# Kernel tuning notes

Hardware: AMD Instinct MI355X
Metric: run time of the kernel (lower is better)

The kernel has to match this reference:

```python
import jax, jax.numpy as jnp
import numpy as np

B, T, IN, H, OUT, HOR = 512, 720, 6, 128, 3, 360


def _cell(xin, h, c, Wih, Whh, bih, bhh):
    # PyTorch LSTM gate order: i, f, g, o
    g = xin @ Wih.T + h @ Whh.T + bih + bhh
    i, f, gg, o = jnp.split(g, 4, axis=-1)
    c = jax.nn.sigmoid(f) * c + jax.nn.sigmoid(i) * jnp.tanh(gg)
    h = jax.nn.sigmoid(o) * jnp.tanh(c)
    return h, c


def _run_layer(x, Wih, Whh, bih, bhh, reverse):
    xs = x[:, ::-1] if reverse else x
    # hoist input projection out of the scan: (B,T,4H)
    pre = jnp.einsum('bti,gi->btg', xs, Wih) + bih + bhh
    h0 = jnp.zeros((x.shape[0], Whh.shape[1]), x.dtype)

    def step(carry, gt):
        h, c = carry
        g = gt + h @ Whh.T
        i, f, gg, o = jnp.split(g, 4, axis=-1)
        c = jax.nn.sigmoid(f) * c + jax.nn.sigmoid(i) * jnp.tanh(gg)
        h = jax.nn.sigmoid(o) * jnp.tanh(c)
        return (h, c), h

    (hT, cT), ys = jax.lax.scan(step, (h0, h0), jnp.swapaxes(pre, 0, 1))
    ys = jnp.swapaxes(ys, 0, 1)
    if reverse:
        ys = ys[:, ::-1]
    return ys, hT, cT


def reference(x, e0f_Wih, e0f_Whh, e0f_bih, e0f_bhh, e0b_Wih, e0b_Whh, e0b_bih, e0b_bhh,
              e1f_Wih, e1f_Whh, e1f_bih, e1f_bhh, e1b_Wih, e1b_Whh, e1b_bih, e1b_bhh,
              brh_W, brh_b, brc_W, brc_b,
              d0_Wih, d0_Whh, d0_bih, d0_bhh, d1_Wih, d1_Whh, d1_bih, d1_bhh,
              out_W, out_b, start_token):
    b = x.shape[0]
    # bidirectional encoder, layer 0 (input_dim -> H per direction)
    y0f, h0f, c0f = _run_layer(x, e0f_Wih, e0f_Whh, e0f_bih, e0f_bhh, False)
    y0b, h0b, c0b = _run_layer(x, e0b_Wih, e0b_Whh, e0b_bih, e0b_bhh, True)
    y0 = jnp.concatenate([y0f, y0b], axis=-1)  # (B,T,2H)
    # layer 1 (2H -> H per direction); dropout inactive in eval
    _, h1f, c1f = _run_layer(y0, e1f_Wih, e1f_Whh, e1f_bih, e1f_bhh, False)
    _, h1b, c1b = _run_layer(y0, e1b_Wih, e1b_Whh, e1b_bih, e1b_bhh, True)
    # (num_layers, B, 2H): cat fwd/bwd final states per layer
    h_enc = jnp.stack([jnp.concatenate([h0f, h0b], -1), jnp.concatenate([h1f, h1b], -1)])
    c_enc = jnp.stack([jnp.concatenate([c0f, c0b], -1), jnp.concatenate([c1f, c1b], -1)])
    h_dec = h_enc @ brh_W.T + brh_b  # (2,B,H)
    c_dec = c_enc @ brc_W.T + brc_b
    xin0 = jnp.broadcast_to(start_token[0, 0], (b, start_token.shape[-1]))  # (B,3)

    def dec_step(carry, _):
        h0, c0, h1, c1, xin = carry
        h0, c0 = _cell(xin, h0, c0, d0_Wih, d0_Whh, d0_bih, d0_bhh)
        h1, c1 = _cell(h0, h1, c1, d1_Wih, d1_Whh, d1_bih, d1_bhh)
        pred = h1 @ out_W.T + out_b
        return (h0, c0, h1, c1, pred), pred

    carry0 = (h_dec[0], c_dec[0], h_dec[1], c_dec[1], xin0)
    _, preds = jax.lax.scan(dec_step, carry0, None, length=HOR)  # (HOR,B,3)
    return jnp.swapaxes(preds, 0, 1)  # (B,HOR,3)


def setup_inputs() -> dict:
    ks = iter(jax.random.split(jax.random.key(0), 40))

    def p(shape, s=0.05):
        return jax.random.normal(next(ks), shape, dtype=jnp.float32) * s

    d = {"x": jax.random.normal(next(ks), (B, T, IN), dtype=jnp.float32)}
    for name, ind in (("e0f", IN), ("e0b", IN), ("e1f", 2 * H), ("e1b", 2 * H)):
        d[name + "_Wih"] = p((4 * H, ind))
        d[name + "_Whh"] = p((4 * H, H))
        d[name + "_bih"] = p((4 * H,))
        d[name + "_bhh"] = p((4 * H,))
    d["brh_W"] = p((H, 2 * H)); d["brh_b"] = p((H,))
    d["brc_W"] = p((H, 2 * H)); d["brc_b"] = p((H,))
    for name, ind in (("d0", OUT), ("d1", H)):
        d[name + "_Wih"] = p((4 * H, ind))
        d[name + "_Whh"] = p((4 * H, H))
        d[name + "_bih"] = p((4 * H,))
        d[name + "_bhh"] = p((4 * H,))
    d["out_W"] = p((OUT, H)); d["out_b"] = p((OUT,))
    d["start_token"] = p((1, 1, OUT), 0.01)
    return d
```

## Files before the change

kernel.cpp:

```cpp
#include <hip/hip_runtime.h>

typedef __attribute__((ext_vector_type(8))) short bf16x8;
typedef __attribute__((ext_vector_type(4))) float f32x4;

#define MFMA16(a,b,c) __builtin_amdgcn_mfma_f32_16x16x32_bf16((a),(b),(c),0,0,0)

#define T_SEQ  720
#define NB     512
#define HD     128
#define GD     512
#define BT     16
#define HP     136
#define HP0    168
#define YT     256
#define WLP    68
#define HORZ   360

__device__ __forceinline__ float bf2f_(unsigned short u){
  union { unsigned int i; float f; } v; v.i = ((unsigned int)u) << 16; return v.f;
}
__device__ __forceinline__ unsigned short f2bf(float f){
  union { float f; unsigned int i; } v; v.f = f;
  unsigned int r = v.i + 0x7fffu + ((v.i >> 16) & 1u);
  return (unsigned short)(r >> 16);
}
__device__ __forceinline__ float rcp_(float x){ return __builtin_amdgcn_rcpf(x); }
__device__ __forceinline__ float sigm(float x){ return rcp_(1.f + __expf(-x)); }
__device__ __forceinline__ float tanh_(float x){
  return __builtin_fmaf(2.f, rcp_(1.f + __expf(-2.f * x)), -1.f);
}
__device__ __forceinline__ bf16x8 cvt8(const float* p){
  bf16x8 r;
  #pragma unroll
  for (int i = 0; i < 8; ++i) r[i] = (short)f2bf(p[i]);
  return r;
}
__device__ __forceinline__ void gl_lds16(const unsigned short* g, unsigned short* l){
  __builtin_amdgcn_global_load_lds(
      (const __attribute__((address_space(1))) void*)(g),
      (__attribute__((address_space(3))) void*)(l), 16, 0, 0);
}

__global__ __launch_bounds__(512, 2)
void enc_layer0_kernel(const float* __restrict__ x,
                       const float* __restrict__ WihF, const float* __restrict__ WhhF,
                       const float* __restrict__ bihF, const float* __restrict__ bhhF,
                       const float* __restrict__ WihB, const float* __restrict__ WhhB,
                       const float* __restrict__ bihB, const float* __restrict__ bhhB,
                       unsigned short* __restrict__ y0,
                       float* __restrict__ ench, float* __restrict__ encc)
{
  __shared__ __align__(16) unsigned short h_buf[2][BT * HP0];
  const int tid  = threadIdx.x;
  const int lane = tid & 63;
  const int w    = tid >> 6;
  const int l15  = lane & 15;
  const int q    = lane >> 4;
  const int dir  = blockIdx.x >> 5;
  const int bbase = (blockIdx.x & 31) * BT;

  const float* Wih = dir ? WihB : WihF;
  const float* Whh = dir ? WhhB : WhhF;
  const float* bih = dir ? bihB : bihF;
  const float* bhh = dir ? bhhB : bhhF;

  bf16x8 bw[4][5];
  f32x4  bias_vec[4];
  #pragma unroll
  for (int g = 0; g < 4; ++g) {
    const int n = g * 128 + w * 16 + l15;
    #pragma unroll
    for (int kt = 0; kt < 4; ++kt)
      bw[g][kt] = cvt8(Whh + n * HD + kt * 32 + q * 8);
    bf16x8 f;
    #pragma unroll
    for (int j = 0; j < 8; ++j) {
      const int kk = q * 8 + j;
      float wv = 0.f;
      if (kk < 6)       wv = Wih[n * 6 + kk];
      else if (kk < 12) wv = Wih[n * 6 + (kk - 6)];
      f[j] = (short)f2bf(wv);
    }
    bw[g][4] = f;
    const float b = bih[n] + bhh[n];
    bias_vec[g][0] = b; bias_vec[g][1] = b; bias_vec[g][2] = b; bias_vec[g][3] = b;
  }

  int t = dir ? (T_SEQ - 1) : 0;
  const int dt = dir ? -1 : 1;
  const int xr_ = tid / 6, xk_ = tid % 6;

  float cst[4] = {0.f, 0.f, 0.f, 0.f};
  for (int i = tid; i < 2 * BT * HP0; i += 512) (&h_buf[0][0])[i] = 0;
  __syncthreads();
  float xv_cur = 0.f;
  if (tid < 96) {
    const float v0 = x[((size_t)(bbase + xr_) * T_SEQ + t) * 6 + xk_];
    const unsigned short hi = f2bf(v0);
    h_buf[0][xr_ * HP0 + 128 + xk_] = hi;
    h_buf[0][xr_ * HP0 + 134 + xk_] = f2bf(v0 - bf2f_(hi));
    xv_cur = x[((size_t)(bbase + xr_) * T_SEQ + t + dt) * 6 + xk_];
  }
  __syncthreads();

  for (int s = 0; s < T_SEQ; ++s, t += dt) {
    const int cur = s & 1, nxt = cur ^ 1;

    if (s > 0 && tid < 256) {
      const int b = tid >> 4, c8 = tid & 15;
      const bf16x8 hv = *reinterpret_cast<const bf16x8*>(&h_buf[cur][b * HP0 + c8 * 8]);
      *reinterpret_cast<bf16x8*>(y0 + ((size_t)(bbase + b) * T_SEQ + (t - dt)) * 256 + dir * HD + c8 * 8) = hv;
    }
    float xv_next = 0.f;
    if (tid < 96 && s + 2 < T_SEQ)
      xv_next = x[((size_t)(bbase + xr_) * T_SEQ + (t + 2 * dt)) * 6 + xk_];

    f32x4 acc[4];
    #pragma unroll
    for (int kt = 0; kt < 5; ++kt) {
      const bf16x8 af = *reinterpret_cast<const bf16x8*>(&h_buf[cur][l15 * HP0 + kt * 32 + q * 8]);
      #pragma unroll
      for (int g = 0; g < 4; ++g)
        acc[g] = MFMA16(af, bw[g][kt], kt == 0 ? bias_vec[g] : acc[g]);
    }

    #pragma unroll
    for (int r = 0; r < 4; ++r) {
      const float i_ = acc[0][r], f_ = acc[1][r], g_ = acc[2][r], o_ = acc[3][r];
      const float c_ = sigm(f_) * cst[r] + sigm(i_) * tanh_(g_);
      cst[r] = c_;
      const float h_ = sigm(o_) * tanh_(c_);
      h_buf[nxt][(q * 4 + r) * HP0 + w * 16 + l15] = f2bf(h_);
      if (s == T_SEQ - 1) {
        const int b   = bbase + q * 4 + r;
        const int cix = w * 16 + l15;
        ench[(dir * NB + b) * HD + cix] = h_;
        encc[(dir * NB + b) * HD + cix] = c_;
      }
    }
    if (tid < 96 && s + 1 < T_SEQ) {
      const unsigned short hi = f2bf(xv_cur);
      h_buf[nxt][xr_ * HP0 + 128 + xk_] = hi;
      h_buf[nxt][xr_ * HP0 + 134 + xk_] = f2bf(xv_cur - bf2f_(hi));
    }
    xv_cur = xv_next;
    __syncthreads();
  }
  if (tid < 256) {
    const int cur = T_SEQ & 1;
    const int b = tid >> 4, c8 = tid & 15;
    const bf16x8 hv = *reinterpret_cast<const bf16x8*>(&h_buf[cur][b * HP0 + c8 * 8]);
    const int tl = dir ? 0 : (T_SEQ - 1);
    *reinterpret_cast<bf16x8*>(y0 + ((size_t)(bbase + b) * T_SEQ + tl) * 256 + dir * HD + c8 * 8) = hv;
  }
}

#define ENC1_YPART(ACC, YB)                                                    \
  {                                                                            \
    _Pragma("unroll")                                                          \
    for (int g = 0; g < 4; ++g) {                                              \
      (ACC)[g][0] = bias[g]; (ACC)[g][1] = bias[g];                            \
      (ACC)[g][2] = bias[g]; (ACC)[g][3] = bias[g];                            \
    }                                                                          \
    _Pragma("unroll")                                                          \
    for (int kt = 0; kt < 2; ++kt) {                                           \
      const int swz_ = ((kt * 4 + q) & 15) ^ l15;                              \
      const bf16x8 af = *reinterpret_cast<const bf16x8*>(&(YB)[l15 * YT + swz_ * 8]); \
      _Pragma("unroll")                                                        \
      for (int g = 0; g < 4; ++g) {                                            \
        const bf16x8 bl = *reinterpret_cast<const bf16x8*>(&wlds[nofs[g] + kt * 32 + q * 8]); \
        (ACC)[g] = MFMA16(af, bl, (ACC)[g]);                                   \
      }                                                                        \
    }                                                                          \
    _Pragma("unroll")                                                          \
    for (int kt = 2; kt < 8; ++kt) {                                           \
      const int c_ = kt * 4 + q;                                               \
      const int swz_ = (c_ & 16) | ((c_ & 15) ^ l15);                          \
      const bf16x8 af = *reinterpret_cast<const bf16x8*>(&(YB)[l15 * YT + swz_ * 8]); \
      _Pragma("unroll")                                                        \
      for (int g = 0; g < 4; ++g) (ACC)[g] = MFMA16(af, bw[g][kt - 2], (ACC)[g]); \
    }                                                                          \
  }

#define ENC1_BODY(S, CUR, NXT, ACCC, ACCN)                                     \
  {                                                                            \
    if ((S) + 2 < T_SEQ)                                                       \
      gl_lds16(y0 + grow + (size_t)(t + 2 * dt) * 256, b2 + w * 512);          \
    _Pragma("unroll")                                                          \
    for (int kt = 8; kt < 12; ++kt) {                                          \
      const bf16x8 af = *reinterpret_cast<const bf16x8*>(&h_buf[CUR][l15 * HP + (kt - 8) * 32 + q * 8]); \
      _Pragma("unroll")                                                        \
      for (int g = 0; g < 4; ++g) (ACCC)[g] = MFMA16(af, bw[g][kt - 2], (ACCC)[g]); \
    }                                                                          \
    if ((S) + 1 < T_SEQ) ENC1_YPART(ACCN, b1)                                  \
    _Pragma("unroll")                                                          \
    for (int r = 0; r < 4; ++r) {                                              \
      const float i_ = (ACCC)[0][r], f_ = (ACCC)[1][r];                        \
      const float g_ = (ACCC)[2][r], o_ = (ACCC)[3][r];                        \
      const float cc_ = sigm(f_) * cst[r] + sigm(i_) * tanh_(g_);              \
      cst[r] = cc_;                                                            \
      const float h_ = sigm(o_) * tanh_(cc_);                                  \
      h_buf[NXT][(q * 4 + r) * HP + w * 16 + l15] = f2bf(h_);                  \
      if ((S) == T_SEQ - 1) {                                                  \
        const int b_ = bbase + q * 4 + r;                                      \
        const int cix = w * 16 + l15;                                          \
        ench[(dir * NB + b_) * HD + cix] = h_;                                 \
        encc[(dir * NB + b_) * HD + cix] = cc_;                                \
      }                                                                        \
    }                                                                          \
    { unsigned short* tmp_ = b0; b0 = b1; b1 = b2; b2 = tmp_; }                \
    t += dt;                                                                   \
    __syncthreads();                                                           \
  }

__global__ __launch_bounds__(512, 2)
void enc_layer1_kernel(const unsigned short* __restrict__ y0,
                       const float* __restrict__ WihF, const float* __restrict__ WhhF,
                       const float* __restrict__ bihF, const float* __restrict__ bhhF,
                       const float* __restrict__ WihB, const float* __restrict__ WhhB,
                       const float* __restrict__ bihB, const float* __restrict__ bhhB,
                       float* __restrict__ ench, float* __restrict__ encc)
{
  __shared__ __align__(16) unsigned short wlds[GD * WLP];
  __shared__ __align__(16) unsigned short ybuf[3][BT * YT];
  __shared__ __align__(16) unsigned short h_buf[2][BT * HP];

  const int tid  = threadIdx.x;
  const int lane = tid & 63;
  const int w    = tid >> 6;
  const int l15  = lane & 15;
  const int q    = lane >> 4;
  const int dir  = blockIdx.x >> 5;
  const int bbase = (blockIdx.x & 31) * BT;

  const float* Wih = dir ? WihB : WihF;
  const float* Whh = dir ? WhhB : WhhF;
  const float* bih = dir ? bihB : bihF;
  const float* bhh = dir ? bhhB : bhhF;

  for (int i = tid; i < GD * 8; i += 512) {
    const int n = i >> 3, c8 = i & 7;
    *reinterpret_cast<bf16x8*>(&wlds[n * WLP + c8 * 8]) = cvt8(Wih + n * 256 + c8 * 8);
  }

  bf16x8 bw[4][10];
  float  bias[4];
  int    nofs[4];
  #pragma unroll
  for (int g = 0; g < 4; ++g) {
    const int n = g * 128 + w * 16 + l15;
    nofs[g] = n * WLP;
    #pragma unroll
    for (int kt = 2; kt < 8; ++kt)  bw[g][kt - 2] = cvt8(Wih + n * 256 + kt * 32 + q * 8);
    #pragma unroll
    for (int kt = 8; kt < 12; ++kt) bw[g][kt - 2] = cvt8(Whh + n * HD + (kt - 8) * 32 + q * 8);
    bias[g] = bih[n] + bhh[n];
  }

  const int sb   = 2 * w + (lane >> 5);
  const int cimg = lane & 31;
  const int sig  = (cimg & 16) | ((cimg & 15) ^ (sb & 15));
  const size_t grow = (size_t)(bbase + sb) * T_SEQ * 256 + (size_t)sig * 8;
  unsigned short* b0 = &ybuf[0][0];
  unsigned short* b1 = &ybuf[1][0];
  unsigned short* b2 = &ybuf[2][0];

  int t = dir ? (T_SEQ - 1) : 0;
  const int dt = dir ? -1 : 1;

  float cst[4] = {0.f, 0.f, 0.f, 0.f};
  for (int i = tid; i < 2 * BT * HP; i += 512) (&h_buf[0][0])[i] = 0;
  gl_lds16(y0 + grow + (size_t)t * 256,        b0 + w * 512);
  gl_lds16(y0 + grow + (size_t)(t + dt) * 256, b1 + w * 512);
  __syncthreads();

  f32x4 accP[4], accQ[4];
  ENC1_YPART(accP, b0)

  for (int m = 0; m < T_SEQ / 2; ++m) {
    const int s0 = 2 * m;
    ENC1_BODY(s0,     0, 1, accP, accQ)
    ENC1_BODY(s0 + 1, 1, 0, accQ, accP)
  }
}

__global__ void bridge_kernel(const float* __restrict__ ench0, const float* __restrict__ encc0,
                              const float* __restrict__ ench1, const float* __restrict__ encc1,
                              const float* __restrict__ brhW, const float* __restrict__ brhb,
                              const float* __restrict__ brcW, const float* __restrict__ brcb,
                              float* __restrict__ dech, float* __restrict__ decc)
{
  const int idx = blockIdx.x * 256 + threadIdx.x;
  const int sel = idx >> 17;
  const int l   = (idx >> 16) & 1;
  const int b   = (idx >> 7) & 511;
  const int j   = idx & 127;
  const float* W  = sel ? brcW : brhW;
  const float* bb = sel ? brcb : brhb;
  const float* s0 = sel ? (l ? encc1 : encc0) : (l ? ench1 : ench0);
  float a = bb[j];
  for (int k = 0; k < 128; ++k) a += W[j * 256 + k] * s0[b * 128 + k];
  for (int k = 0; k < 128; ++k) a += W[j * 256 + 128 + k] * s0[(512 + b) * 128 + k];
  float* dst = sel ? decc : dech;
  dst[(l * 512 + b) * 128 + j] = a;
}

__global__ __launch_bounds__(512, 2)
void decoder_kernel(const float* __restrict__ dech, const float* __restrict__ decc,
                    const float* __restrict__ W0ih, const float* __restrict__ W0hh,
                    const float* __restrict__ b0ih, const float* __restrict__ b0hh,
                    const float* __restrict__ W1ih, const float* __restrict__ W1hh,
                    const float* __restrict__ b1ih, const float* __restrict__ b1hh,
                    const float* __restrict__ outW, const float* __restrict__ outb,
                    const float* __restrict__ stok,
                    float* __restrict__ out)
{
  __shared__ __align__(16) unsigned short w0lds[GD * WLP];
  __shared__ __align__(16) unsigned short w1lds[GD * WLP];
  __shared__ __align__(16) unsigned short h0_buf[2][BT * HP];
  __shared__ __align__(16) unsigned short h1_buf[2][BT * HP];
  __shared__ __align__(16) unsigned short xstage[8][BT * 8];
  __shared__ __align__(16) unsigned short xzero[8];

  const int tid  = threadIdx.x;
  const int lane = tid & 63;
  const int w    = tid >> 6;
  const int l15  = lane & 15;
  const int q    = lane >> 4;
  const int bbase = blockIdx.x * BT;

  for (int i = tid; i < GD * 8; i += 512) {
    const int n = i >> 3, c8 = i & 7;
    *reinterpret_cast<bf16x8*>(&w0lds[n * WLP + c8 * 8]) = cvt8(W0hh + n * HD + c8 * 8);
    *reinterpret_cast<bf16x8*>(&w1lds[n * WLP + c8 * 8]) = cvt8(W1ih + n * HD + c8 * 8);
  }

  bf16x8 bw0[4][2];
  bf16x8 bw1[4][6];
  bf16x8 wx0[4];
  f32x4  bias0_vec[4], bias1_vec[4];
  int    nofs[4];
  #pragma unroll
  for (int g = 0; g < 4; ++g) {
    const int n = g * 128 + w * 16 + l15;
    nofs[g] = n * WLP;
    #pragma unroll
    for (int kt = 2; kt < 4; ++kt) {
      bw0[g][kt - 2] = cvt8(W0hh + n * HD + kt * 32 + q * 8);
      bw1[g][kt - 2] = cvt8(W1ih + n * HD + kt * 32 + q * 8);
    }
    #pragma unroll
    for (int kt = 4; kt < 8; ++kt)
      bw1[g][kt - 2] = cvt8(W1hh + n * HD + (kt - 4) * 32 + q * 8);
    bf16x8 f;
    #pragma unroll
    for (int j = 0; j < 8; ++j) {
      const int kk = q * 8 + j;
      f[j] = (short)((kk < 3) ? f2bf(W0ih[n * 3 + kk]) : 0);
    }
    wx0[g] = f;
    const float b0 = b0ih[n] + b0hh[n];
    const float b1 = b1ih[n] + b1hh[n];
    bias0_vec[g][0] = b0; bias0_vec[g][1] = b0; bias0_vec[g][2] = b0; bias0_vec[g][3] = b0;
    bias1_vec[g][0] = b1; bias1_vec[g][1] = b1; bias1_vec[g][2] = b1; bias1_vec[g][3] = b1;
  }

  bf16x8 owf[4];
  float outb_s = 0.f;
  {
    bf16x8 z;
    #pragma unroll
    for (int i = 0; i < 8; ++i) z[i] = 0;
    #pragma unroll
    for (int kt = 0; kt < 4; ++kt) owf[kt] = z;
    if (l15 < 3) {
      #pragma unroll
      for (int kt = 0; kt < 4; ++kt) owf[kt] = cvt8(outW + l15 * HD + kt * 32 + q * 8);
      outb_s = outb[l15];
    }
  }

  float c0[4], c1[4];
  #pragma unroll
  for (int r = 0; r < 4; ++r) {
    const int b   = bbase + q * 4 + r;
    const int cix = w * 16 + l15;
    c0[r] = decc[b * HD + cix];
    c1[r] = decc[(NB + b) * HD + cix];
  }
  for (int i = tid; i < BT * HD; i += 512) {
    const int b = i >> 7, cix = i & 127;
    h0_buf[0][b * HP + cix] = f2bf(dech[(bbase + b) * HD + cix]);
    h1_buf[0][b * HP + cix] = f2bf(dech[(NB + bbase + b) * HD + cix]);
  }
  {
    const int row = lane >> 2, col = lane & 3;
    const unsigned short v = (col < 3) ? f2bf(stok[col]) : 0;
    xstage[w][row * 8 + col] = v;
    xstage[w][row * 8 + 4 + col] = 0;
    if (tid < 8) xzero[tid] = 0;
  }
  const unsigned short* afx_ptr = (q == 0) ? &xstage[w][l15 * 8] : xzero;
  __syncthreads();

  for (int s = 0; s < HORZ; ++s) {
    const int cur = s & 1, nxt = cur ^ 1;

    f32x4 accC[4];
    #pragma unroll
    for (int kt = 4; kt < 8; ++kt) {
      const bf16x8 af = *reinterpret_cast<const bf16x8*>(&h1_buf[cur][l15 * HP + (kt - 4) * 32 + q * 8]);
      #pragma unroll
      for (int g = 0; g < 4; ++g)
        accC[g] = MFMA16(af, bw1[g][kt - 2], kt == 4 ? bias1_vec[g] : accC[g]);
    }
    f32x4 p = {0.f, 0.f, 0.f, 0.f};
    #pragma unroll
    for (int kt = 0; kt < 4; ++kt) {
      const bf16x8 af = *reinterpret_cast<const bf16x8*>(&h1_buf[cur][l15 * HP + kt * 32 + q * 8]);
      p = MFMA16(af, owf[kt], p);
    }
    f32x4 acc0[4];
    #pragma unroll
    for (int kt = 0; kt < 2; ++kt) {
      const bf16x8 af = *reinterpret_cast<const bf16x8*>(&h0_buf[cur][l15 * HP + kt * 32 + q * 8]);
      #pragma unroll
      for (int g = 0; g < 4; ++g) {
        const bf16x8 bl = *reinterpret_cast<const bf16x8*>(&w0lds[nofs[g] + kt * 32 + q * 8]);
        acc0[g] = MFMA16(af, bl, kt == 0 ? bias0_vec[g] : acc0[g]);
      }
    }
    #pragma unroll
    for (int kt = 2; kt < 4; ++kt) {
      const bf16x8 af = *reinterpret_cast<const bf16x8*>(&h0_buf[cur][l15 * HP + kt * 32 + q * 8]);
      #pragma unroll
      for (int g = 0; g < 4; ++g) acc0[g] = MFMA16(af, bw0[g][kt - 2], acc0[g]);
    }
    if (l15 < 3) {
      #pragma unroll
      for (int r = 0; r < 4; ++r) {
        const float v = p[r] + outb_s;
        xstage[w][(q * 4 + r) * 8 + l15] = f2bf(v);
        if (w == 0 && s > 0)
          out[((size_t)(bbase + q * 4 + r) * HORZ + (s - 1)) * 3 + l15] = v;
      }
    }
    {
      const bf16x8 afx = *reinterpret_cast<const bf16x8*>(afx_ptr);
      #pragma unroll
      for (int g = 0; g < 4; ++g) acc0[g] = MFMA16(afx, wx0[g], acc0[g]);
    }
    #pragma unroll
    for (int r = 0; r < 4; ++r) {
      const float i_ = acc0[0][r], f_ = acc0[1][r], g_ = acc0[2][r], o_ = acc0[3][r];
      const float c_ = sigm(f_) * c0[r] + sigm(i_) * tanh_(g_);
      c0[r] = c_;
      const float h_ = sigm(o_) * tanh_(c_);
      h0_buf[nxt][(q * 4 + r) * HP + w * 16 + l15] = f2bf(h_);
    }
    __syncthreads();

    #pragma unroll
    for (int kt = 0; kt < 2; ++kt) {
      const bf16x8 af = *reinterpret_cast<const bf16x8*>(&h0_buf[nxt][l15 * HP + kt * 32 + q * 8]);
      #pragma unroll
      for (int g = 0; g < 4; ++g) {
        const bf16x8 bl = *reinterpret_cast<const bf16x8*>(&w1lds[nofs[g] + kt * 32 + q * 8]);
        accC[g] = MFMA16(af, bl, accC[g]);
      }
    }
    #pragma unroll
    for (int kt = 2; kt < 4; ++kt) {
      const bf16x8 af = *reinterpret_cast<const bf16x8*>(&h0_buf[nxt][l15 * HP + kt * 32 + q * 8]);
      #pragma unroll
      for (int g = 0; g < 4; ++g) accC[g] = MFMA16(af, bw1[g][kt - 2], accC[g]);
    }
    #pragma unroll
    for (int r = 0; r < 4; ++r) {
      const float i_ = accC[0][r], f_ = accC[1][r], g_ = accC[2][r], o_ = accC[3][r];
      const float c_ = sigm(f_) * c1[r] + sigm(i_) * tanh_(g_);
      c1[r] = c_;
      const float h_ = sigm(o_) * tanh_(c_);
      h1_buf[nxt][(q * 4 + r) * HP + w * 16 + l15] = f2bf(h_);
    }
    __syncthreads();
  }

  {
    const int cur = HORZ & 1;
    f32x4 p = {0.f, 0.f, 0.f, 0.f};
    #pragma unroll
    for (int kt = 0; kt < 4; ++kt) {
      const bf16x8 af = *reinterpret_cast<const bf16x8*>(&h1_buf[cur][l15 * HP + kt * 32 + q * 8]);
      p = MFMA16(af, owf[kt], p);
    }
    if (w == 0 && l15 < 3) {
      #pragma unroll
      for (int r = 0; r < 4; ++r)
        out[((size_t)(bbase + q * 4 + r) * HORZ + (HORZ - 1)) * 3 + l15] = p[r] + outb_s;
    }
  }
}

extern "C" void kernel_launch(void* const* d_in, const int* in_sizes, int n_in,
                              void* d_out, int out_size, void* d_ws, size_t ws_size,
                              hipStream_t stream)
{
  (void)in_sizes; (void)n_in; (void)out_size; (void)ws_size;
  const float* x      = (const float*)d_in[0];
  const float* e0fWih = (const float*)d_in[1];
  const float* e0fWhh = (const float*)d_in[2];
  const float* e0fbih = (const float*)d_in[3];
  const float* e0fbhh = (const float*)d_in[4];
  const float* e0bWih = (const float*)d_in[5];
  const float* e0bWhh = (const float*)d_in[6];
  const float* e0bbih = (const float*)d_in[7];
  const float* e0bbhh = (const float*)d_in[8];
  const float* e1fWih = (const float*)d_in[9];
  const float* e1fWhh = (const float*)d_in[10];
  const float* e1fbih = (const float*)d_in[11];
  const float* e1fbhh = (const float*)d_in[12];
  const float* e1bWih = (const float*)d_in[13];
  const float* e1bWhh = (const float*)d_in[14];
  const float* e1bbih = (const float*)d_in[15];
  const float* e1bbhh = (const float*)d_in[16];
  const float* brhW   = (const float*)d_in[17];
  const float* brhb   = (const float*)d_in[18];
  const float* brcW   = (const float*)d_in[19];
  const float* brcb   = (const float*)d_in[20];
  const float* d0Wih  = (const float*)d_in[21];
  const float* d0Whh  = (const float*)d_in[22];
  const float* d0bih  = (const float*)d_in[23];
  const float* d0bhh  = (const float*)d_in[24];
  const float* d1Wih  = (const float*)d_in[25];
  const float* d1Whh  = (const float*)d_in[26];
  const float* d1bih  = (const float*)d_in[27];
  const float* d1bhh  = (const float*)d_in[28];
  const float* outW   = (const float*)d_in[29];
  const float* outb   = (const float*)d_in[30];
  const float* stok   = (const float*)d_in[31];

  char* ws = (char*)d_ws;
  unsigned short* y0 = (unsigned short*)ws;
  size_t off = (size_t)NB * T_SEQ * 256 * sizeof(unsigned short);
  const size_t blk = (size_t)2 * NB * HD * sizeof(float);
  float* ench0 = (float*)(ws + off); off += blk;
  float* encc0 = (float*)(ws + off); off += blk;
  float* ench1 = (float*)(ws + off); off += blk;
  float* encc1 = (float*)(ws + off); off += blk;
  float* dech  = (float*)(ws + off); off += blk;
  float* decc  = (float*)(ws + off); off += blk;

  enc_layer0_kernel<<<dim3(64), dim3(512), 0, stream>>>(
      x, e0fWih, e0fWhh, e0fbih, e0fbhh, e0bWih, e0bWhh, e0bbih, e0bbhh,
      y0, ench0, encc0);
  enc_layer1_kernel<<<dim3(64), dim3(512), 0, stream>>>(
      y0, e1fWih, e1fWhh, e1fbih, e1fbhh, e1bWih, e1bWhh, e1bbih, e1bbhh,
      ench1, encc1);
  bridge_kernel<<<dim3(1024), dim3(256), 0, stream>>>(
      ench0, encc0, ench1, encc1, brhW, brhb, brcW, brcb, dech, decc);
  decoder_kernel<<<dim3(32), dim3(512), 0, stream>>>(
      dech, decc, d0Wih, d0Whh, d0bih, d0bhh, d1Wih, d1Whh, d1bih, d1bhh,
      outW, outb, stok, (float*)d_out);
}
```

Baseline: 3.146 ms.

## Compute decoder feedback input via shuffles and scalar FMAs instead of LDS MFMA

The decoder now broadcasts each step's 3-wide prediction to all lanes with warp shuffles and folds the input projection into the accumulator init as scalar FMAs. This replaces the xstage LDS staging buffer and the extra MFMA on a mostly-zero operand. It also moves the output projection to the end of each step, so the h1 recurrent MFMAs follow the layer-0 barrier instead of preceding it. The trade is fewer registers and one less LDS round-trip, against shuffle latency and a longer serial chain after the second barrier.

After: 2.893 ms (median of 2 runs). -8.0%, faster.

```diff
diff --git a/kernel.cpp b/kernel.cpp
--- a/kernel.cpp
+++ b/kernel.cpp
@@ -319,8 +319,6 @@
   __shared__ __align__(16) unsigned short w1lds[GD * WLP];
   __shared__ __align__(16) unsigned short h0_buf[2][BT * HP];
   __shared__ __align__(16) unsigned short h1_buf[2][BT * HP];
-  __shared__ __align__(16) unsigned short xstage[8][BT * 8];
-  __shared__ __align__(16) unsigned short xzero[8];
 
   const int tid  = threadIdx.x;
   const int lane = tid & 63;
@@ -337,8 +335,7 @@
 
   bf16x8 bw0[4][2];
   bf16x8 bw1[4][6];
-  bf16x8 wx0[4];
-  f32x4  bias0_vec[4], bias1_vec[4];
+  float  xw0[4][3], bias0[4], bias1[4];
   int    nofs[4];
   #pragma unroll
   for (int g = 0; g < 4; ++g) {
@@ -352,17 +349,10 @@
     #pragma unroll
     for (int kt = 4; kt < 8; ++kt)
       bw1[g][kt - 2] = cvt8(W1hh + n * HD + (kt - 4) * 32 + q * 8);
-    bf16x8 f;
-    #pragma unroll
-    for (int j = 0; j < 8; ++j) {
-      const int kk = q * 8 + j;
-      f[j] = (short)((kk < 3) ? f2bf(W0ih[n * 3 + kk]) : 0);
-    }
-    wx0[g] = f;
-    const float b0 = b0ih[n] + b0hh[n];
-    const float b1 = b1ih[n] + b1hh[n];
-    bias0_vec[g][0] = b0; bias0_vec[g][1] = b0; bias0_vec[g][2] = b0; bias0_vec[g][3] = b0;
-    bias1_vec[g][0] = b1; bias1_vec[g][1] = b1; bias1_vec[g][2] = b1; bias1_vec[g][3] = b1;
+    #pragma unroll
+    for (int k = 0; k < 3; ++k) xw0[g][k] = W0ih[n * 3 + k];
+    bias0[g] = b0ih[n] + b0hh[n];
+    bias1[g] = b1ih[n] + b1hh[n];
   }
 
   bf16x8 owf[4];
@@ -393,66 +383,41 @@
     h0_buf[0][b * HP + cix] = f2bf(dech[(bbase + b) * HD + cix]);
     h1_buf[0][b * HP + cix] = f2bf(dech[(NB + bbase + b) * HD + cix]);
   }
+  float xr[4][3];
   {
-    const int row = lane >> 2, col = lane & 3;
-    const unsigned short v = (col < 3) ? f2bf(stok[col]) : 0;
-    xstage[w][row * 8 + col] = v;
-    xstage[w][row * 8 + 4 + col] = 0;
-    if (tid < 8) xzero[tid] = 0;
-  }
-  const unsigned short* afx_ptr = (q == 0) ? &xstage[w][l15 * 8] : xzero;
+    const float s0 = stok[0], s1 = stok[1], s2 = stok[2];
+    #pragma unroll
+    for (int r = 0; r < 4; ++r) { xr[r][0] = s0; xr[r][1] = s1; xr[r][2] = s2; }
+  }
   __syncthreads();
 
   for (int s = 0; s < HORZ; ++s) {
     const int cur = s & 1, nxt = cur ^ 1;
 
-    f32x4 accC[4];
-    #pragma unroll
-    for (int kt = 4; kt < 8; ++kt) {
-      const bf16x8 af = *reinterpret_cast<const bf16x8*>(&h1_buf[cur][l15 * HP + (kt - 4) * 32 + q * 8]);
-      #pragma unroll
-      for (int g = 0; g < 4; ++g)
-        accC[g] = MFMA16(af, bw1[g][kt - 2], kt == 4 ? bias1_vec[g] : accC[g]);
-    }
-    f32x4 p = {0.f, 0.f, 0.f, 0.f};
-    #pragma unroll
-    for (int kt = 0; kt < 4; ++kt) {
-      const bf16x8 af = *reinterpret_cast<const bf16x8*>(&h1_buf[cur][l15 * HP + kt * 32 + q * 8]);
-      p = MFMA16(af, owf[kt], p);
-    }
-    f32x4 acc0[4];
+    f32x4 acc[4];
+    #pragma unroll
+    for (int g = 0; g < 4; ++g)
+      #pragma unroll
+      for (int r = 0; r < 4; ++r)
+        acc[g][r] = bias0[g] + xw0[g][0] * xr[r][0] + xw0[g][1] * xr[r][1] + xw0[g][2] * xr[r][2];
     #pragma unroll
     for (int kt = 0; kt < 2; ++kt) {
       const bf16x8 af = *reinterpret_cast<const bf16x8*>(&h0_buf[cur][l15 * HP + kt * 32 + q * 8]);
       #pragma unroll
       for (int g = 0; g < 4; ++g) {
         const bf16x8 bl = *reinterpret_cast<const bf16x8*>(&w0lds[nofs[g] + kt * 32 + q * 8]);
-        acc0[g] = MFMA16(af, bl, kt == 0 ? bias0_vec[g] : acc0[g]);
+        acc[g] = MFMA16(af, bl, acc[g]);
       }
     }
     #pragma unroll
     for (int kt = 2; kt < 4; ++kt) {
       const bf16x8 af = *reinterpret_cast<const bf16x8*>(&h0_buf[cur][l15 * HP + kt * 32 + q * 8]);
       #pragma unroll
-      for (int g = 0; g < 4; ++g) acc0[g] = MFMA16(af, bw0[g][kt - 2], acc0[g]);
-    }
-    if (l15 < 3) {
-      #pragma unroll
-      for (int r = 0; r < 4; ++r) {
-        const float v = p[r] + outb_s;
-        xstage[w][(q * 4 + r) * 8 + l15] = f2bf(v);
-        if (w == 0 && s > 0)
-          out[((size_t)(bbase + q * 4 + r) * HORZ + (s - 1)) * 3 + l15] = v;
-      }
-    }
-    {
-      const bf16x8 afx = *reinterpret_cast<const bf16x8*>(afx_ptr);
-      #pragma unroll
-      for (int g = 0; g < 4; ++g) acc0[g] = MFMA16(afx, wx0[g], acc0[g]);
+      for (int g = 0; g < 4; ++g) acc[g] = MFMA16(af, bw0[g][kt - 2], acc[g]);
     }
     #pragma unroll
     for (int r = 0; r < 4; ++r) {
-      const float i_ = acc0[0][r], f_ = acc0[1][r], g_ = acc0[2][r], o_ = acc0[3][r];
+      const float i_ = acc[0][r], f_ = acc[1][r], g_ = acc[2][r], o_ = acc[3][r];
       const float c_ = sigm(f_) * c0[r] + sigm(i_) * tanh_(g_);
       c0[r] = c_;
       const float h_ = sigm(o_) * tanh_(c_);
@@ -461,44 +426,60 @@
     __syncthreads();
 
     #pragma unroll
+    for (int g = 0; g < 4; ++g) {
+      acc[g][0] = bias1[g]; acc[g][1] = bias1[g];
+      acc[g][2] = bias1[g]; acc[g][3] = bias1[g];
+    }
+    #pragma unroll
     for (int kt = 0; kt < 2; ++kt) {
       const bf16x8 af = *reinterpret_cast<const bf16x8*>(&h0_buf[nxt][l15 * HP + kt * 32 + q * 8]);
       #pragma unroll
       for (int g = 0; g < 4; ++g) {
         const bf16x8 bl = *reinterpret_cast<const bf16x8*>(&w1lds[nofs[g] + kt * 32 + q * 8]);
-        accC[g] = MFMA16(af, bl, accC[g]);
+        acc[g] = MFMA16(af, bl, acc[g]);
       }
     }
     #pragma unroll
     for (int kt = 2; kt < 4; ++kt) {
       const bf16x8 af = *reinterpret_cast<const bf16x8*>(&h0_buf[nxt][l15 * HP + kt * 32 + q * 8]);
       #pragma unroll
-      for (int g = 0; g < 4; ++g) accC[g] = MFMA16(af, bw1[g][kt - 2], accC[g]);
+      for (int g = 0; g < 4; ++g) acc[g] = MFMA16(af, bw1[g][kt - 2], acc[g]);
+    }
+    #pragma unroll
+    for (int kt = 4; kt < 8; ++kt) {
+      const bf16x8 af = *reinterpret_cast<const bf16x8*>(&h1_buf[cur][l15 * HP + (kt - 4) * 32 + q * 8]);
+      #pragma unroll
+      for (int g = 0; g < 4; ++g) acc[g] = MFMA16(af, bw1[g][kt - 2], acc[g]);
     }
     #pragma unroll
     for (int r = 0; r < 4; ++r) {
-      const float i_ = accC[0][r], f_ = accC[1][r], g_ = accC[2][r], o_ = accC[3][r];
+      const float i_ = acc[0][r], f_ = acc[1][r], g_ = acc[2][r], o_ = acc[3][r];
       const float c_ = sigm(f_) * c1[r] + sigm(i_) * tanh_(g_);
       c1[r] = c_;
       const float h_ = sigm(o_) * tanh_(c_);
       h1_buf[nxt][(q * 4 + r) * HP + w * 16 + l15] = f2bf(h_);
     }
     __syncthreads();
-  }
-
-  {
-    const int cur = HORZ & 1;
+
     f32x4 p = {0.f, 0.f, 0.f, 0.f};
     #pragma unroll
     for (int kt = 0; kt < 4; ++kt) {
-      const bf16x8 af = *reinterpret_cast<const bf16x8*>(&h1_buf[cur][l15 * HP + kt * 32 + q * 8]);
+      const bf16x8 af = *reinterpret_cast<const bf16x8*>(&h1_buf[nxt][l15 * HP + kt * 32 + q * 8]);
       p = MFMA16(af, owf[kt], p);
     }
+    float pb[4];
+    #pragma unroll
+    for (int r = 0; r < 4; ++r) pb[r] = p[r] + outb_s;
     if (w == 0 && l15 < 3) {
       #pragma unroll
       for (int r = 0; r < 4; ++r)
-        out[((size_t)(bbase + q * 4 + r) * HORZ + (HORZ - 1)) * 3 + l15] = p[r] + outb_s;
-    }
+        out[((size_t)(bbase + q * 4 + r) * HORZ + s) * 3 + l15] = pb[r];
+    }
+    #pragma unroll
+    for (int r = 0; r < 4; ++r)
+      #pragma unroll
+      for (int c = 0; c < 3; ++c)
+        xr[r][c] = __shfl(pb[r], (q << 4) + c, 64);
   }
 }
 
```
